# Optimization experiments

Measured on AMD Instinct MI355X. Metric: run time of the kernel, lower is better.

## Reference

```python
import jax, jax.numpy as jnp
import numpy as np

B, F, V, D = 16384, 16, 100000, 16  # batch, n_fields, vocab, embed_dim; dims = F*D = 256
EPS = 1e-5


def _bn(x, g, b):
    # torch.nn.BatchNorm1d in training mode: biased batch variance
    m = x.mean(0)
    v = x.var(0)
    return g * (x - m) * jax.lax.rsqrt(v + EPS) + b


def setup_inputs() -> dict:
    ks = iter(jax.random.split(jax.random.key(0), 40))

    def rn(shape, s=0.05):
        return jax.random.normal(next(ks), shape, jnp.float32) * s

    return {
        "feat_ids": jax.random.randint(next(ks), (B, F), 0, V, jnp.int32),
        "domain_ids": jax.random.randint(next(ks), (B,), 0, 3, jnp.int32),
        "emb": rn((F, V, D), 0.1),
        "hW0": rn((256, 128)), "hb0": jnp.zeros(128), "hg0": jnp.ones(128), "hbe0": jnp.zeros(128),
        "hW1": rn((128, 64)), "hb1": jnp.zeros(64), "hg1": jnp.ones(64), "hbe1": jnp.zeros(64),
        "hW2": rn((64, 1024)), "hb2": jnp.zeros(1024), "hg2": jnp.ones(1024), "hbe2": jnp.zeros(1024),
        "cw": rn((3, 256)), "cb": jnp.zeros((3, 256)),
        "mW0": rn((256, 512)), "mb0": jnp.zeros(512), "mg0": jnp.ones(512), "mbe0": jnp.zeros(512),
        "mW1": rn((512, 256)), "mb1": jnp.zeros(256), "mg1": jnp.ones(256), "mbe1": jnp.zeros(256),
        "u0": rn((256, 32)), "u1": rn((32, 32)), "v0": rn((32, 32)), "v1": rn((32, 256)),
        "ab0": jnp.zeros(32), "ab1": jnp.zeros(256),
        "gamma1": jnp.ones(256), "bias1": jnp.zeros(256),
        "lw": rn((512,)), "lb": jnp.zeros(1),
    }


def _forward(feat_ids, emb, hW0, hb0, hg0, hbe0, hW1, hb1, hg1, hbe1,
             hW2, hb2, hg2, hbe2, cw, cb, mW0, mb0, mg0, mbe0,
             mW1, mb1, mg1, mbe1, u0, u1, v0, v1, ab0, ab1,
             gamma1, bias1, lw, lb):
    b, f = feat_ids.shape
    # EmbeddingLayer(squeeze_dim=True): per-field lookup then concat -> [B, F*D]
    e = emb[jnp.arange(f)[None, :], feat_ids].reshape(b, -1)
    h = e
    for W, bb, g, be in ((hW0, hb0, hg0, hbe0), (hW1, hb1, hg1, hbe1), (hW2, hb2, hg2, hbe2)):
        h = jax.nn.relu(_bn(h @ W + bb, g, be))
    k = u1.shape[0]
    H = h.reshape(b, k, k)  # [B, k, k]
    # CrossNetwork: x_{l+1} = x0 * (x_l . w_l) + b_l + x_l
    x = e
    for i in range(cw.shape[0]):
        x = e * (x @ cw[i])[:, None] + cb[i] + x
    cn_out = x  # [B, 256]
    m = e
    for W, bb, g, be in ((mW0, mb0, mg0, mbe0), (mW1, mb1, mg1, mbe1)):
        m = jax.nn.relu(_bn(m @ W + bb, g, be))
    # hyper low-rank adapter: einsum('mi,bij,jn->bmn') applied lazily so the
    # [B,256,32] per-sample weight is never materialized (associativity)
    t = jax.nn.sigmoid(jnp.einsum('bi,bij->bj', m @ u0, H) @ v0 + ab0)   # [B, 32]
    t = jnp.einsum('bi,bij->bj', t @ u1, H) @ v1 + ab1                    # [B, 256]
    mu = t.mean(0)
    var = t.var(0, ddof=1)  # torch.var default is unbiased
    m = gamma1 * (t - mu) / jnp.sqrt(var + EPS) + bias1 + m  # norm + residual
    y = jnp.concatenate([cn_out, m], axis=1) @ lw + lb[0]     # LR head
    # Every domain branch computes identical values (shared weights, full-batch
    # input, dropout p=0), so the torch.where domain-select is the identity.
    return jax.nn.sigmoid(y)  # [B]


def reference(feat_ids, domain_ids, emb, hW0, hb0, hg0, hbe0, hW1, hb1, hg1, hbe1,
              hW2, hb2, hg2, hbe2, cw, cb, mW0, mb0, mg0, mbe0,
              mW1, mb1, mg1, mbe1, u0, u1, v0, v1, ab0, ab1,
              gamma1, bias1, lw, lb):
    return _forward(feat_ids, emb, hW0, hb0, hg0, hbe0, hW1, hb1, hg1, hbe1,
                    hW2, hb2, hg2, hbe2, cw, cb, mW0, mb0, mg0, mbe0,
                    mW1, mb1, mg1, mbe1, u0, u1, v0, v1, ab0, ab1,
                    gamma1, bias1, lw, lb)
```

## Files before the change

kernel.cpp:

```cpp
#include <hip/hip_runtime.h>

typedef unsigned short u16;
typedef __attribute__((ext_vector_type(8))) short bf16x8;
typedef __attribute__((ext_vector_type(4))) float f32x4;
#define BATCH 16384

__device__ __forceinline__ float b2f(u16 u){ unsigned int i=((unsigned int)u)<<16; float f; __builtin_memcpy(&f,&i,4); return f; }
__device__ __forceinline__ u16 f2b(float f){ unsigned int x; __builtin_memcpy(&x,&f,4); unsigned int r=(x + 0x7fffu + ((x>>16)&1u))>>16; return (u16)r; }

__global__ __launch_bounds__(256) void prep_kernel(float* __restrict__ S,
                                                   const float* __restrict__ hb0, const float* __restrict__ mb0,
                                                   float* __restrict__ catb,
                                                   const float* __restrict__ w0, const float* __restrict__ w1,
                                                   const float* __restrict__ w2, const float* __restrict__ w3,
                                                   const float* __restrict__ w4, const float* __restrict__ w5,
                                                   const float* __restrict__ w6,
                                                   u16* __restrict__ catWt, u16* __restrict__ t1,
                                                   u16* __restrict__ t2, u16* __restrict__ t4,
                                                   u16* __restrict__ t5, u16* __restrict__ t6,
                                                   const int* __restrict__ ids,
                                                   const float* __restrict__ emb,
                                                   u16* __restrict__ e){
  int blk = blockIdx.x;
  int tid = threadIdx.x;
  if (blk < 18){
    int i = blk*256 + tid;
    if (i < 4480) S[i] = 0.f;
  } else if (blk == 18){
    for (int i = tid; i < 640; i += 256) catb[i] = (i < 128) ? hb0[i] : mb0[i-128];
  } else if (blk < 1523){
    int c = blk - 19;
    if (c < 640){        int idx=c*256+tid;        int n=idx>>8, k=idx&255;
                         catWt[idx] = f2b(n<128 ? w0[k*128+n] : w3[k*512+(n-128)]); }
    else if (c < 672){   int idx=(c-640)*256+tid;  t1[idx]=f2b(w1[(idx%128)*64   + idx/128]); }
    else if (c < 928){   int idx=(c-672)*256+tid;  t2[idx]=f2b(w2[(idx%64)*1024  + idx/64]);  }
    else if (c < 1440){  int idx=(c-928)*256+tid;  t4[idx]=f2b(w4[(idx%512)*256  + idx/512]); }
    else if (c < 1472){  int idx=(c-1440)*256+tid; t5[idx]=f2b(w5[(idx%256)*32   + idx/256]); }
    else {               int idx=(c-1472)*256+tid; t6[idx]=f2b(w6[(idx%32)*256   + idx/32]);  }
  } else {
    int g = blk - 1523;
    int b = g*16 + (tid >> 4), f = tid & 15;
    int id = ids[b*16 + f];
    const float4* src = (const float4*)(emb + ((size_t)f*100000 + (size_t)id)*16);
    float4 v0 = src[0], v1 = src[1], v2 = src[2], v3 = src[3];
    u16 o[16] = { f2b(v0.x),f2b(v0.y),f2b(v0.z),f2b(v0.w), f2b(v1.x),f2b(v1.y),f2b(v1.z),f2b(v1.w),
                  f2b(v2.x),f2b(v2.y),f2b(v2.z),f2b(v2.w), f2b(v3.x),f2b(v3.y),f2b(v3.z),f2b(v3.w) };
    uint4 p0, p1; __builtin_memcpy(&p0, &o[0], 16); __builtin_memcpy(&p1, &o[8], 16);
    uint4* dst = (uint4*)(e + (size_t)b*256 + f*16);
    dst[0] = p0; dst[1] = p1;
  }
}

template<int BK>
__device__ __forceinline__ void gemm_body(const u16* __restrict__ A,
                                          const u16* __restrict__ Wt,
                                          const float* __restrict__ bias,
                                          u16* __restrict__ Ca,
                                          u16* __restrict__ Cb,
                                          int Nsplit,
                                          const float* __restrict__ asums,
                                          const float* __restrict__ asumsq,
                                          const float* __restrict__ ag,
                                          const float* __restrict__ abe,
                                          float* __restrict__ sums,
                                          float* __restrict__ sumsq,
                                          int N, int K, int n0, int m0,
                                          u16* lds, float* bnS, float* bnB){
  constexpr int STR = BK + 8;
  constexpr int EPT = BK/4;
  u16* As = lds;
  u16* Bs = lds + 64*STR;
  int tid = threadIdx.x;
  int lane = tid & 63, w = tid >> 6, quad = lane >> 4, m16 = lane & 15;
  int srow = tid >> 2, skoff = (tid & 3)*EPT;
  if (asums != nullptr){
    for (int k = tid; k < K; k += 256){
      float mean = asums[k] * (1.f/(float)BATCH);
      float var  = asumsq[k] * (1.f/(float)BATCH) - mean*mean;
      float sc   = ag[k] * rsqrtf(var + 1e-5f);
      bnS[k] = sc;
      bnB[k] = abe[k] - mean*sc;
    }
    __syncthreads();
  }
  f32x4 acc[4] = {};
  int ng = n0 + srow;
  uint4 a0, a1, b0, b1;
  {
    const u16* ap = A + (size_t)(m0+srow)*K + skoff;
    a0 = *(const uint4*)ap;
    if (EPT == 16) a1 = *(const uint4*)(ap + 8);
    if (ng < N){
      const u16* bp = Wt + (size_t)ng*K + skoff;
      b0 = *(const uint4*)bp;
      if (EPT == 16) b1 = *(const uint4*)(bp + 8);
    } else { b0 = make_uint4(0u,0u,0u,0u); b1 = b0; }
  }
  for (int k0 = 0; k0 < K; k0 += BK){
    u16 at[EPT];
    __builtin_memcpy(at, &a0, 16);
    if (EPT == 16) __builtin_memcpy(at+8, &a1, 16);
    if (asums != nullptr){
#pragma unroll
      for (int j=0;j<EPT;j++){
        float v = b2f(at[j]) * bnS[k0+skoff+j] + bnB[k0+skoff+j];
        at[j] = f2b(v > 0.f ? v : 0.f);
      }
    }
    uint4 s0, s1;
    __builtin_memcpy(&s0, at, 16);
    *(uint4*)&As[srow*STR + skoff] = s0;
    if (EPT == 16){ __builtin_memcpy(&s1, at+8, 16); *(uint4*)&As[srow*STR + skoff + 8] = s1; }
    *(uint4*)&Bs[srow*STR + skoff] = b0;
    if (EPT == 16) *(uint4*)&Bs[srow*STR + skoff + 8] = b1;
    if (k0 + BK < K){
      const u16* ap = A + (size_t)(m0+srow)*K + k0 + BK + skoff;
      a0 = *(const uint4*)ap;
      if (EPT == 16) a1 = *(const uint4*)(ap + 8);
      if (ng < N){
        const u16* bp = Wt + (size_t)ng*K + k0 + BK + skoff;
        b0 = *(const uint4*)bp;
        if (EPT == 16) b1 = *(const uint4*)(bp + 8);
      }
    }
    __syncthreads();
#pragma unroll
    for (int sub=0; sub<BK/32; sub++){
      bf16x8 bfrag = *(bf16x8*)&Bs[(w*16 + m16)*STR + sub*32 + quad*8];
#pragma unroll
      for (int mc=0;mc<4;mc++){
        bf16x8 afrag = *(bf16x8*)&As[(mc*16 + m16)*STR + sub*32 + quad*8];
        acc[mc] = __builtin_amdgcn_mfma_f32_16x16x32_bf16(afrag, bfrag, acc[mc], 0, 0, 0);
      }
    }
    __syncthreads();
  }
  int cw = n0 + w*16 + m16;
  float bvv = (bias != nullptr && cw < N) ? bias[cw] : 0.f;
  float cs = 0.f, cq = 0.f;
  u16* Cs = lds;
#pragma unroll
  for (int mc=0;mc<4;mc++)
#pragma unroll
    for (int r=0;r<4;r++){
      float v = acc[mc][r] + bvv;
      cs += v; cq += v*v;
      Cs[(mc*16 + quad*4 + r)*72 + w*16 + m16] = f2b(v);
    }
  if (sums != nullptr){
    cs += __shfl_xor(cs, 16, 64); cs += __shfl_xor(cs, 32, 64);
    cq += __shfl_xor(cq, 16, 64); cq += __shfl_xor(cq, 32, 64);
    if (quad == 0 && cw < N){ atomicAdd(&sums[cw], cs); atomicAdd(&sumsq[cw], cq); }
  }
  __syncthreads();
  int row = tid >> 2, c4 = (tid & 3)*16;
  int cg = n0 + c4;
  if (cg < N){
    u16* outp; int stride, colbase;
    if (Cb != nullptr && n0 >= Nsplit){ outp = Cb; stride = N - Nsplit; colbase = cg - Nsplit; }
    else if (Cb != nullptr){            outp = Ca; stride = Nsplit;     colbase = cg; }
    else {                              outp = Ca; stride = N;          colbase = cg; }
    uint4 p0 = *(uint4*)&Cs[row*72 + c4];
    uint4 p1 = *(uint4*)&Cs[row*72 + c4 + 8];
    *(uint4*)(outp + (size_t)(m0+row)*stride + colbase) = p0;
    *(uint4*)(outp + (size_t)(m0+row)*stride + colbase + 8) = p1;
  }
}

template<int BK>
__global__ __launch_bounds__(256) void gemm_mfma(const u16* __restrict__ A,
                                                 const u16* __restrict__ Wt,
                                                 const float* __restrict__ bias,
                                                 u16* __restrict__ Ca,
                                                 u16* __restrict__ Cb,
                                                 int Nsplit,
                                                 const float* __restrict__ asums,
                                                 const float* __restrict__ asumsq,
                                                 const float* __restrict__ ag,
                                                 const float* __restrict__ abe,
                                                 float* __restrict__ sums,
                                                 float* __restrict__ sumsq,
                                                 int N, int K){
  constexpr int STR = BK + 8;
  __shared__ u16 lds[64*STR*2];
  __shared__ float bnS[512], bnB[512];
  gemm_body<BK>(A, Wt, bias, Ca, Cb, Nsplit, asums, asumsq, ag, abe,
                sums, sumsq, N, K, blockIdx.x*64, blockIdx.y*64, lds, bnS, bnB);
}

__global__ __launch_bounds__(256) void gemm_dual(
    const u16* __restrict__ A1, const u16* __restrict__ Wt1, const float* __restrict__ b1,
    u16* __restrict__ C1,
    const float* __restrict__ as1, const float* __restrict__ aq1,
    const float* __restrict__ g1v, const float* __restrict__ be1,
    float* __restrict__ s1, float* __restrict__ q1, int N1, int K1, int nb1, int nblk1,
    const u16* __restrict__ A2, const u16* __restrict__ Wt2, const float* __restrict__ b2,
    u16* __restrict__ C2,
    const float* __restrict__ as2, const float* __restrict__ aq2,
    const float* __restrict__ g2v, const float* __restrict__ be2,
    float* __restrict__ s2, float* __restrict__ q2, int N2, int K2, int nblk2){
  constexpr int STR = 64 + 8;
  __shared__ u16 lds[64*STR*2];
  __shared__ float bnS[512], bnB[512];
  int blk = blockIdx.x;
  if (blk < nb1){
    int n0 = (blk % nblk1)*64, m0 = (blk / nblk1)*64;
    gemm_body<64>(A1, Wt1, b1, C1, nullptr, 0, as1, aq1, g1v, be1,
                  s1, q1, N1, K1, n0, m0, lds, bnS, bnB);
  } else {
    int q = blk - nb1;
    int n0 = (q % nblk2)*64, m0 = (q / nblk2)*64;
    gemm_body<64>(A2, Wt2, b2, C2, nullptr, 0, as2, aq2, g2v, be2,
                  s2, q2, N2, K2, n0, m0, lds, bnS, bnB);
  }
}

#define HSTR 1056
__global__ __launch_bounds__(512) void adapter_core(const u16* __restrict__ H,
                                                    const u16* __restrict__ Mout,
                                                    const u16* __restrict__ u0t,
                                                    const float* __restrict__ v0,
                                                    const float* __restrict__ u1,
                                                    const float* __restrict__ ab0,
                                                    const float* __restrict__ hsums,
                                                    const float* __restrict__ hsumsq,
                                                    const float* __restrict__ hg,
                                                    const float* __restrict__ hbe,
                                                    const float* __restrict__ msums,
                                                    const float* __restrict__ msumsq,
                                                    const float* __restrict__ mg,
                                                    const float* __restrict__ mbe,
                                                    u16* __restrict__ Z2){
  __shared__ __align__(16) u16 Hs[16*HSTR];
  __shared__ float bnS[1024], bnB[1024];
  __shared__ __align__(8) u16 v0s[1024], u1s[1024];
  __shared__ float mS[256], mB[256];
  __shared__ float PT[512], QS[512];
  __shared__ float ab0s[32];
  int tid = threadIdx.x;
  int r = tid >> 5, j = tid & 31;
  size_t row0 = (size_t)blockIdx.x * 16;
  u16* aS = Hs;

  for (int k = tid; k < 1024; k += 512){
    float mean = hsums[k] * (1.f/(float)BATCH);
    float var  = hsumsq[k] * (1.f/(float)BATCH) - mean*mean;
    float sc   = hg[k] * rsqrtf(var + 1e-5f);
    bnS[k] = sc; bnB[k] = hbe[k] - mean*sc;
  }
  if (tid < 256){
    float4 a = *(const float4*)(v0 + tid*4);
    ushort4 pa = { f2b(a.x), f2b(a.y), f2b(a.z), f2b(a.w) };
    *(ushort4*)&v0s[tid*4] = pa;
    float4 b4 = *(const float4*)(u1 + tid*4);
    ushort4 pb = { f2b(b4.x), f2b(b4.y), f2b(b4.z), f2b(b4.w) };
    *(ushort4*)&u1s[tid*4] = pb;
  } else {
    int c = tid - 256;
    float mean = msums[c] * (1.f/(float)BATCH);
    float var  = msumsq[c] * (1.f/(float)BATCH) - mean*mean;
    float sc   = mg[c] * rsqrtf(var + 1e-5f);
    mS[c] = sc; mB[c] = mbe[c] - mean*sc;
  }
  {
    int el = tid*8;
    uint4 mv = *(const uint4*)(Mout + row0*256 + el);
    *(uint4*)&aS[el] = mv;
  }
  if (tid < 32) ab0s[tid] = ab0[tid];
  __syncthreads();

  {
    int el = tid*8, col = el & 255;
    u16 mt[8]; __builtin_memcpy(mt, &aS[el], 16);
#pragma unroll
    for (int q=0;q<8;q++){
      float v = b2f(mt[q]) * mS[col+q] + mB[col+q];
      mt[q] = f2b(v > 0.f ? v : 0.f);
    }
    uint4 so; __builtin_memcpy(&so, mt, 16);
    *(uint4*)&aS[el] = so;
  }
  __syncthreads();

  {
    float acc = 0.f;
    for (int k8 = 0; k8 < 256; k8 += 8){
      uint4 vu = *(const uint4*)(u0t + j*256 + k8);
      uint4 va; __builtin_memcpy(&va, &aS[r*256 + k8], 16);
      u16 ta[8], tu[8]; __builtin_memcpy(ta, &va, 16); __builtin_memcpy(tu, &vu, 16);
#pragma unroll
      for (int q=0;q<8;q++) acc += b2f(ta[q]) * b2f(tu[q]);
    }
    PT[tid] = acc;
  }
  __syncthreads();

#pragma unroll
  for (int it=0; it<4; it++){
    int el = it*4096 + tid*8;
    int rr = el >> 10, col = el & 1023;
    uint4 hv = *(const uint4*)(H + row0*1024 + el);
    u16 ht[8]; __builtin_memcpy(ht, &hv, 16);
#pragma unroll
    for (int q=0;q<8;q++){
      float v = b2f(ht[q]) * bnS[col+q] + bnB[col+q];
      ht[q] = f2b(v > 0.f ? v : 0.f);
    }
    uint4 so; __builtin_memcpy(&so, ht, 16);
    *(uint4*)&Hs[rr*HSTR + col] = so;
  }
  __syncthreads();

  float acc = 0.f;
#pragma unroll
  for (int i=0;i<32;i++) acc += PT[r*32+i] * b2f(Hs[r*HSTR + i*32 + j]);
  QS[tid] = acc;
  __syncthreads();
  acc = ab0s[j];
#pragma unroll
  for (int i=0;i<32;i++) acc += QS[r*32+i] * b2f(v0s[i*32+j]);
  PT[tid] = 1.f / (1.f + __expf(-acc));
  __syncthreads();
  acc = 0.f;
#pragma unroll
  for (int i=0;i<32;i++) acc += PT[r*32+i] * b2f(u1s[i*32+j]);
  QS[tid] = acc;
  __syncthreads();
  acc = 0.f;
#pragma unroll
  for (int i=0;i<32;i++) acc += QS[r*32+i] * b2f(Hs[r*HSTR + i*32 + j]);
  Z2[(row0 + r)*32 + j] = f2b(acc);
}

__global__ __launch_bounds__(256) void final_kernel(const u16* __restrict__ e,
                                                    const float* __restrict__ cw,
                                                    const float* __restrict__ cb,
                                                    const u16* __restrict__ t,
                                                    const u16* __restrict__ mo,
                                                    const float* __restrict__ tsums,
                                                    const float* __restrict__ tsumsq,
                                                    const float* __restrict__ tg,
                                                    const float* __restrict__ tbe,
                                                    const float* __restrict__ msums,
                                                    const float* __restrict__ msumsq,
                                                    const float* __restrict__ mg,
                                                    const float* __restrict__ mbe,
                                                    const float* __restrict__ lw,
                                                    const float* __restrict__ lb,
                                                    float* __restrict__ out){
  __shared__ float tS[256], tB[256], mS[256], mB[256];
  int tid = threadIdx.x;
  {
    int c = tid;
    float mean = tsums[c] * (1.f/(float)BATCH);
    float var  = (tsumsq[c] - mean*mean*(float)BATCH) * (1.f/(float)(BATCH-1));
    float sc   = tg[c] * rsqrtf(var + 1e-5f);
    tS[c] = sc; tB[c] = tbe[c] - mean*sc;
    float mmean = msums[c] * (1.f/(float)BATCH);
    float mvar  = msumsq[c] * (1.f/(float)BATCH) - mmean*mmean;
    float msc   = mg[c] * rsqrtf(mvar + 1e-5f);
    mS[c] = msc; mB[c] = mbe[c] - mmean*msc;
  }
  __syncthreads();
  int wave = tid >> 6, lane = tid & 63;
  int b = blockIdx.x*4 + wave;
  int n4 = lane*4;
  ushort4 ev = *(const ushort4*)(e + (size_t)b*256 + n4);
  float ec[4] = { b2f(ev.x), b2f(ev.y), b2f(ev.z), b2f(ev.w) };
  float x[4]  = { ec[0], ec[1], ec[2], ec[3] };
  for (int i=0;i<3;i++){
    float p = 0.f;
#pragma unroll
    for (int q=0;q<4;q++) p += x[q] * cw[i*256 + n4 + q];
#pragma unroll
    for (int o=1;o<64;o<<=1) p += __shfl_xor(p, o, 64);
#pragma unroll
    for (int q=0;q<4;q++) x[q] = ec[q]*p + cb[i*256 + n4 + q] + x[q];
  }
  ushort4 tv = *(const ushort4*)(t  + (size_t)b*256 + n4);
  ushort4 mv = *(const ushort4*)(mo + (size_t)b*256 + n4);
  float ta[4] = { b2f(tv.x), b2f(tv.y), b2f(tv.z), b2f(tv.w) };
  float ma[4] = { b2f(mv.x), b2f(mv.y), b2f(mv.z), b2f(mv.w) };
  float p = 0.f;
#pragma unroll
  for (int q=0;q<4;q++){
    int n = n4 + q;
    p += x[q] * lw[n];
    float mr = ma[q]*mS[n] + mB[n];
    mr = mr > 0.f ? mr : 0.f;
    float mf = tS[n]*ta[q] + tB[n] + mr;
    p += mf * lw[256 + n];
  }
#pragma unroll
  for (int o=32;o>0;o>>=1) p += __shfl_down(p, o, 64);
  if (lane == 0){
    float y = p + lb[0];
    out[b] = 1.f / (1.f + __expf(-y));
  }
}

extern "C" void kernel_launch(void* const* d_in, const int* in_sizes, int n_in,
                              void* d_out, int out_size, void* d_ws, size_t ws_size,
                              hipStream_t stream) {
  const int B = BATCH;
  const int*   feat = (const int*)d_in[0];
  const float* emb  = (const float*)d_in[2];
  const float* hW0 = (const float*)d_in[3],  *hb0 = (const float*)d_in[4],  *hg0 = (const float*)d_in[5],  *hbe0 = (const float*)d_in[6];
  const float* hW1 = (const float*)d_in[7],  *hb1 = (const float*)d_in[8],  *hg1 = (const float*)d_in[9],  *hbe1 = (const float*)d_in[10];
  const float* hW2 = (const float*)d_in[11], *hb2 = (const float*)d_in[12], *hg2 = (const float*)d_in[13], *hbe2 = (const float*)d_in[14];
  const float* cw  = (const float*)d_in[15], *cb  = (const float*)d_in[16];
  const float* mW0 = (const float*)d_in[17], *mb0 = (const float*)d_in[18], *mg0 = (const float*)d_in[19], *mbe0 = (const float*)d_in[20];
  const float* mW1 = (const float*)d_in[21], *mb1 = (const float*)d_in[22], *mg1 = (const float*)d_in[23], *mbe1 = (const float*)d_in[24];
  const float* u0  = (const float*)d_in[25], *u1  = (const float*)d_in[26];
  const float* v0  = (const float*)d_in[27], *v1  = (const float*)d_in[28];
  const float* ab0 = (const float*)d_in[29], *ab1 = (const float*)d_in[30];
  const float* gamma1 = (const float*)d_in[31], *bias1 = (const float*)d_in[32];
  const float* lw  = (const float*)d_in[33], *lb = (const float*)d_in[34];
  float* out = (float*)d_out;

  char* base = (char*)d_ws;
  const size_t MB = 1024*1024;
  u16* H    = (u16*)(base);
  u16* e    = (u16*)(base + 32*MB);
  u16* Y0   = (u16*)(base + 40*MB);
  u16* Y1   = (u16*)(base + 44*MB);
  u16* M0   = (u16*)(base + 48*MB);
  u16* Mout = (u16*)(base + 64*MB);
  u16* T    = (u16*)(base + 72*MB);
  u16* Z2   = (u16*)(base + 80*MB);
  u16* catWt= (u16*)(base + 88*MB);
  u16* hW1t = catWt + 163840;
  u16* hW2t = hW1t + 8192;
  u16* mW1t = hW2t + 65536;
  u16* u0t  = mW1t + 131072;
  u16* v1t  = u0t + 8192;
  float* catb = (float*)(v1t + 8192);
  float* S    = catb + 640;

  prep_kernel<<<2547, 256, 0, stream>>>(S, hb0, mb0, catb,
                                        hW0, hW1, hW2, mW0, mW1, u0, v1,
                                        catWt, hW1t, hW2t, mW1t, u0t, v1t,
                                        feat, emb, e);

  gemm_mfma<64><<<dim3(10, B/64), 256, 0, stream>>>(e, catWt, catb, Y0, M0, 128,
      nullptr, nullptr, nullptr, nullptr, S+0, S+640, 640, 256);

  gemm_dual<<<1280, 256, 0, stream>>>(
      Y0, hW1t, hb1, Y1, S+0, S+640, hg0, hbe0, S+1280, S+1344, 64, 128, 256, 1,
      M0, mW1t, mb1, Mout, S+128, S+768, mg0, mbe0, S+3456, S+3712, 256, 512, 4);

  gemm_mfma<64><<<dim3(16, B/64), 256, 0, stream>>>(Y1, hW2t, hb2, H, nullptr, 0,
      S+1280, S+1344, hg1, hbe1, S+1408, S+2432, 1024, 64);

  adapter_core<<<B/16, 512, 0, stream>>>(H, Mout, u0t, v0, u1, ab0,
      S+1408, S+2432, hg2, hbe2, S+3456, S+3712, mg1, mbe1, Z2);
  gemm_mfma<32><<<dim3(4, B/64), 256, 0, stream>>>(Z2, v1t, ab1, T, nullptr, 0,
      nullptr, nullptr, nullptr, nullptr, S+3968, S+4224, 256, 32);

  final_kernel<<<B/4, 256, 0, stream>>>(e, cw, cb, T, Mout,
      S+3968, S+4224, gamma1, bias1,
      S+3456, S+3712, mg1, mbe1, lw, lb, out);
}
```

Before: 324.3 us.

## Fuse all stages into one persistent cooperative kernel with grid syncs

```diff
diff --git a/kernel.cpp b/kernel.cpp
--- a/kernel.cpp
+++ b/kernel.cpp
@@ -1,55 +1,16 @@
 #include <hip/hip_runtime.h>
+#include <hip/hip_cooperative_groups.h>
+
+namespace cg = cooperative_groups;
 
 typedef unsigned short u16;
 typedef __attribute__((ext_vector_type(8))) short bf16x8;
 typedef __attribute__((ext_vector_type(4))) float f32x4;
 #define BATCH 16384
+#define HSTR 1056
 
 __device__ __forceinline__ float b2f(u16 u){ unsigned int i=((unsigned int)u)<<16; float f; __builtin_memcpy(&f,&i,4); return f; }
 __device__ __forceinline__ u16 f2b(float f){ unsigned int x; __builtin_memcpy(&x,&f,4); unsigned int r=(x + 0x7fffu + ((x>>16)&1u))>>16; return (u16)r; }
-
-__global__ __launch_bounds__(256) void prep_kernel(float* __restrict__ S,
-                                                   const float* __restrict__ hb0, const float* __restrict__ mb0,
-                                                   float* __restrict__ catb,
-                                                   const float* __restrict__ w0, const float* __restrict__ w1,
-                                                   const float* __restrict__ w2, const float* __restrict__ w3,
-                                                   const float* __restrict__ w4, const float* __restrict__ w5,
-                                                   const float* __restrict__ w6,
-                                                   u16* __restrict__ catWt, u16* __restrict__ t1,
-                                                   u16* __restrict__ t2, u16* __restrict__ t4,
-                                                   u16* __restrict__ t5, u16* __restrict__ t6,
-                                                   const int* __restrict__ ids,
-                                                   const float* __restrict__ emb,
-                                                   u16* __restrict__ e){
-  int blk = blockIdx.x;
-  int tid = threadIdx.x;
-  if (blk < 18){
-    int i = blk*256 + tid;
-    if (i < 4480) S[i] = 0.f;
-  } else if (blk == 18){
-    for (int i = tid; i < 640; i += 256) catb[i] = (i < 128) ? hb0[i] : mb0[i-128];
-  } else if (blk < 1523){
-    int c = blk - 19;
-    if (c < 640){        int idx=c*256+tid;        int n=idx>>8, k=idx&255;
-                         catWt[idx] = f2b(n<128 ? w0[k*128+n] : w3[k*512+(n-128)]); }
-    else if (c < 672){   int idx=(c-640)*256+tid;  t1[idx]=f2b(w1[(idx%128)*64   + idx/128]); }
-    else if (c < 928){   int idx=(c-672)*256+tid;  t2[idx]=f2b(w2[(idx%64)*1024  + idx/64]);  }
-    else if (c < 1440){  int idx=(c-928)*256+tid;  t4[idx]=f2b(w4[(idx%512)*256  + idx/512]); }
-    else if (c < 1472){  int idx=(c-1440)*256+tid; t5[idx]=f2b(w5[(idx%256)*32   + idx/256]); }
-    else {               int idx=(c-1472)*256+tid; t6[idx]=f2b(w6[(idx%32)*256   + idx/32]);  }
-  } else {
-    int g = blk - 1523;
-    int b = g*16 + (tid >> 4), f = tid & 15;
-    int id = ids[b*16 + f];
-    const float4* src = (const float4*)(emb + ((size_t)f*100000 + (size_t)id)*16);
-    float4 v0 = src[0], v1 = src[1], v2 = src[2], v3 = src[3];
-    u16 o[16] = { f2b(v0.x),f2b(v0.y),f2b(v0.z),f2b(v0.w), f2b(v1.x),f2b(v1.y),f2b(v1.z),f2b(v1.w),
-                  f2b(v2.x),f2b(v2.y),f2b(v2.z),f2b(v2.w), f2b(v3.x),f2b(v3.y),f2b(v3.z),f2b(v3.w) };
-    uint4 p0, p1; __builtin_memcpy(&p0, &o[0], 16); __builtin_memcpy(&p1, &o[8], 16);
-    uint4* dst = (uint4*)(e + (size_t)b*256 + f*16);
-    dst[0] = p0; dst[1] = p1;
-  }
-}
 
 template<int BK>
 __device__ __forceinline__ void gemm_body(const u16* __restrict__ A,
@@ -167,298 +128,323 @@
   }
 }
 
-template<int BK>
-__global__ __launch_bounds__(256) void gemm_mfma(const u16* __restrict__ A,
-                                                 const u16* __restrict__ Wt,
-                                                 const float* __restrict__ bias,
-                                                 u16* __restrict__ Ca,
-                                                 u16* __restrict__ Cb,
-                                                 int Nsplit,
-                                                 const float* __restrict__ asums,
-                                                 const float* __restrict__ asumsq,
-                                                 const float* __restrict__ ag,
-                                                 const float* __restrict__ abe,
-                                                 float* __restrict__ sums,
-                                                 float* __restrict__ sumsq,
-                                                 int N, int K){
-  constexpr int STR = BK + 8;
-  __shared__ u16 lds[64*STR*2];
-  __shared__ float bnS[512], bnB[512];
-  gemm_body<BK>(A, Wt, bias, Ca, Cb, Nsplit, asums, asumsq, ag, abe,
-                sums, sumsq, N, K, blockIdx.x*64, blockIdx.y*64, lds, bnS, bnB);
-}
-
-__global__ __launch_bounds__(256) void gemm_dual(
-    const u16* __restrict__ A1, const u16* __restrict__ Wt1, const float* __restrict__ b1,
-    u16* __restrict__ C1,
-    const float* __restrict__ as1, const float* __restrict__ aq1,
-    const float* __restrict__ g1v, const float* __restrict__ be1,
-    float* __restrict__ s1, float* __restrict__ q1, int N1, int K1, int nb1, int nblk1,
-    const u16* __restrict__ A2, const u16* __restrict__ Wt2, const float* __restrict__ b2,
-    u16* __restrict__ C2,
-    const float* __restrict__ as2, const float* __restrict__ aq2,
-    const float* __restrict__ g2v, const float* __restrict__ be2,
-    float* __restrict__ s2, float* __restrict__ q2, int N2, int K2, int nblk2){
-  constexpr int STR = 64 + 8;
-  __shared__ u16 lds[64*STR*2];
-  __shared__ float bnS[512], bnB[512];
-  int blk = blockIdx.x;
-  if (blk < nb1){
-    int n0 = (blk % nblk1)*64, m0 = (blk / nblk1)*64;
-    gemm_body<64>(A1, Wt1, b1, C1, nullptr, 0, as1, aq1, g1v, be1,
-                  s1, q1, N1, K1, n0, m0, lds, bnS, bnB);
-  } else {
-    int q = blk - nb1;
-    int n0 = (q % nblk2)*64, m0 = (q / nblk2)*64;
-    gemm_body<64>(A2, Wt2, b2, C2, nullptr, 0, as2, aq2, g2v, be2,
-                  s2, q2, N2, K2, n0, m0, lds, bnS, bnB);
-  }
-}
-
-#define HSTR 1056
-__global__ __launch_bounds__(512) void adapter_core(const u16* __restrict__ H,
-                                                    const u16* __restrict__ Mout,
-                                                    const u16* __restrict__ u0t,
-                                                    const float* __restrict__ v0,
-                                                    const float* __restrict__ u1,
-                                                    const float* __restrict__ ab0,
-                                                    const float* __restrict__ hsums,
-                                                    const float* __restrict__ hsumsq,
-                                                    const float* __restrict__ hg,
-                                                    const float* __restrict__ hbe,
-                                                    const float* __restrict__ msums,
-                                                    const float* __restrict__ msumsq,
-                                                    const float* __restrict__ mg,
-                                                    const float* __restrict__ mbe,
-                                                    u16* __restrict__ Z2){
-  __shared__ __align__(16) u16 Hs[16*HSTR];
-  __shared__ float bnS[1024], bnB[1024];
-  __shared__ __align__(8) u16 v0s[1024], u1s[1024];
-  __shared__ float mS[256], mB[256];
-  __shared__ float PT[512], QS[512];
-  __shared__ float ab0s[32];
-  int tid = threadIdx.x;
-  int r = tid >> 5, j = tid & 31;
-  size_t row0 = (size_t)blockIdx.x * 16;
-  u16* aS = Hs;
-
-  for (int k = tid; k < 1024; k += 512){
-    float mean = hsums[k] * (1.f/(float)BATCH);
-    float var  = hsumsq[k] * (1.f/(float)BATCH) - mean*mean;
-    float sc   = hg[k] * rsqrtf(var + 1e-5f);
-    bnS[k] = sc; bnB[k] = hbe[k] - mean*sc;
-  }
-  if (tid < 256){
-    float4 a = *(const float4*)(v0 + tid*4);
-    ushort4 pa = { f2b(a.x), f2b(a.y), f2b(a.z), f2b(a.w) };
-    *(ushort4*)&v0s[tid*4] = pa;
-    float4 b4 = *(const float4*)(u1 + tid*4);
-    ushort4 pb = { f2b(b4.x), f2b(b4.y), f2b(b4.z), f2b(b4.w) };
-    *(ushort4*)&u1s[tid*4] = pb;
-  } else {
-    int c = tid - 256;
-    float mean = msums[c] * (1.f/(float)BATCH);
-    float var  = msumsq[c] * (1.f/(float)BATCH) - mean*mean;
-    float sc   = mg[c] * rsqrtf(var + 1e-5f);
-    mS[c] = sc; mB[c] = mbe[c] - mean*sc;
-  }
+struct MegaArgs {
+  const int* feat; const float* emb;
+  const float *hb0, *mb0;
+  const float *hW0, *hW1, *hW2, *mW0, *mW1, *u0w, *v1w;
+  const float *hg0, *hbe0, *hb1, *hg1, *hbe1, *hb2, *hg2, *hbe2;
+  const float *mb1, *mg0, *mbe0, *mg1, *mbe1;
+  const float *v0, *u1, *ab0, *ab1, *gamma1, *bias1, *cw, *cb, *lw, *lb;
+  u16 *H, *e, *Y0, *Y1, *M0, *Mout, *T;
+  u16 *catWt, *hW1t, *hW2t, *mW1t, *u0t, *v1t;
+  float *catb, *S, *hSg, *hBg, *mSg, *mBg;
+  float* out;
+};
+
+__global__ __launch_bounds__(256, 4) void mega_kernel(MegaArgs a){
+  __shared__ __align__(16) char smem[23424];
+  cg::grid_group gg = cg::this_grid();
+  const int tid = threadIdx.x;
+  const int bid = blockIdx.x;
+  const int nb  = gridDim.x;
+
   {
-    int el = tid*8;
-    uint4 mv = *(const uint4*)(Mout + row0*256 + el);
-    *(uint4*)&aS[el] = mv;
-  }
-  if (tid < 32) ab0s[tid] = ab0[tid];
-  __syncthreads();
+    int gi = bid*256 + tid;
+    if (gi < 4480) a.S[gi] = 0.f;
+    else if (gi < 5120){ int i = gi - 4480; a.catb[i] = (i < 128) ? a.hb0[i] : a.mb0[i-128]; }
+    for (int c = bid; c < 1504; c += nb){
+      if (c < 640){        int idx=c*256+tid;        int n=idx>>8, k=idx&255;
+                           a.catWt[idx] = f2b(n<128 ? a.hW0[k*128+n] : a.mW0[k*512+(n-128)]); }
+      else if (c < 672){   int idx=(c-640)*256+tid;  a.hW1t[idx]=f2b(a.hW1[(idx%128)*64   + idx/128]); }
+      else if (c < 928){   int idx=(c-672)*256+tid;  a.hW2t[idx]=f2b(a.hW2[(idx%64)*1024  + idx/64]);  }
+      else if (c < 1440){  int idx=(c-928)*256+tid;  a.mW1t[idx]=f2b(a.mW1[(idx%512)*256  + idx/512]); }
+      else if (c < 1472){  int idx=(c-1440)*256+tid; a.u0t[idx]=f2b(a.u0w[(idx%256)*32   + idx/256]); }
+      else {               int idx=(c-1472)*256+tid; a.v1t[idx]=f2b(a.v1w[(idx%32)*256   + idx/32]);  }
+    }
+    for (int g = bid; g < 1024; g += nb){
+      int b = g*16 + (tid >> 4), f = tid & 15;
+      int id = a.feat[b*16 + f];
+      const float4* src = (const float4*)(a.emb + ((size_t)f*100000 + (size_t)id)*16);
+      float4 v0 = src[0], v1 = src[1], v2 = src[2], v3 = src[3];
+      u16 o[16] = { f2b(v0.x),f2b(v0.y),f2b(v0.z),f2b(v0.w), f2b(v1.x),f2b(v1.y),f2b(v1.z),f2b(v1.w),
+                    f2b(v2.x),f2b(v2.y),f2b(v2.z),f2b(v2.w), f2b(v3.x),f2b(v3.y),f2b(v3.z),f2b(v3.w) };
+      uint4 p0, p1; __builtin_memcpy(&p0, &o[0], 16); __builtin_memcpy(&p1, &o[8], 16);
+      uint4* dst = (uint4*)(a.e + (size_t)b*256 + f*16);
+      dst[0] = p0; dst[1] = p1;
+    }
+  }
+  gg.sync();
+
+  u16*  glds = (u16*)smem;
+  float* bnS = (float*)(smem + 18432);
+  float* bnB = (float*)(smem + 18432 + 2048);
+
+  for (int t = bid; t < 2560; t += nb){
+    __syncthreads();
+    gemm_body<64>(a.e, a.catWt, a.catb, a.Y0, a.M0, 128,
+                  nullptr, nullptr, nullptr, nullptr,
+                  a.S+0, a.S+640, 640, 256, (t%10)*64, (t/10)*64, glds, bnS, bnB);
+  }
+  gg.sync();
+
+  for (int t = bid; t < 1280; t += nb){
+    __syncthreads();
+    if (t < 256){
+      gemm_body<64>(a.Y0, a.hW1t, a.hb1, a.Y1, nullptr, 0,
+                    a.S+0, a.S+640, a.hg0, a.hbe0,
+                    a.S+1280, a.S+1344, 64, 128, 0, t*64, glds, bnS, bnB);
+    } else {
+      int q = t - 256;
+      gemm_body<64>(a.M0, a.mW1t, a.mb1, a.Mout, nullptr, 0,
+                    a.S+128, a.S+768, a.mg0, a.mbe0,
+                    a.S+3456, a.S+3712, 256, 512, (q%4)*64, (q/4)*64, glds, bnS, bnB);
+    }
+  }
+  gg.sync();
+
+  for (int t = bid; t < 4096; t += nb){
+    __syncthreads();
+    gemm_body<64>(a.Y1, a.hW2t, a.hb2, a.H, nullptr, 0,
+                  a.S+1280, a.S+1344, a.hg1, a.hbe1,
+                  a.S+1408, a.S+2432, 1024, 64, (t%16)*64, (t/16)*64, glds, bnS, bnB);
+  }
+  gg.sync();
+
+  if (bid < 4){
+    int i = bid*256 + tid;
+    float mean = a.S[1408+i] * (1.f/(float)BATCH);
+    float var  = a.S[2432+i] * (1.f/(float)BATCH) - mean*mean;
+    float sc   = a.hg2[i] * rsqrtf(var + 1e-5f);
+    a.hSg[i] = sc; a.hBg[i] = a.hbe2[i] - mean*sc;
+    if (i < 256){
+      float mmean = a.S[3456+i] * (1.f/(float)BATCH);
+      float mvar  = a.S[3712+i] * (1.f/(float)BATCH) - mmean*mmean;
+      float msc   = a.mg1[i] * rsqrtf(mvar + 1e-5f);
+      a.mSg[i] = msc; a.mBg[i] = a.mbe1[i] - mmean*msc;
+    }
+  }
+  gg.sync();
 
   {
-    int el = tid*8, col = el & 255;
-    u16 mt[8]; __builtin_memcpy(mt, &aS[el], 16);
-#pragma unroll
-    for (int q=0;q<8;q++){
-      float v = b2f(mt[q]) * mS[col+q] + mB[col+q];
-      mt[q] = f2b(v > 0.f ? v : 0.f);
-    }
-    uint4 so; __builtin_memcpy(&so, mt, 16);
-    *(uint4*)&aS[el] = so;
-  }
-  __syncthreads();
+    u16* Hs   = (u16*)smem;
+    u16* v0s  = (u16*)(smem + 16896);
+    u16* u1s  = (u16*)(smem + 18944);
+    float* PT = (float*)(smem + 20992);
+    float* QS = (float*)(smem + 22016);
+    float* ab0s = (float*)(smem + 23040);
+    int r = tid >> 5, j = tid & 31;
+    {
+      float4 av = *(const float4*)(a.v0 + tid*4);
+      ushort4 pa = { f2b(av.x), f2b(av.y), f2b(av.z), f2b(av.w) };
+      *(ushort4*)&v0s[tid*4] = pa;
+      float4 b4 = *(const float4*)(a.u1 + tid*4);
+      ushort4 pb = { f2b(b4.x), f2b(b4.y), f2b(b4.z), f2b(b4.w) };
+      *(ushort4*)&u1s[tid*4] = pb;
+      if (tid < 32) ab0s[tid] = a.ab0[tid];
+    }
+    __syncthreads();
+    for (int t = bid; t < 2048; t += nb){
+      size_t row0 = (size_t)t * 8;
+      const u16* Hb = a.H + row0*1024 + tid*8;
+      uint4 h0 = *(const uint4*)(Hb);
+      uint4 h1 = *(const uint4*)(Hb + 2048);
+      uint4 h2 = *(const uint4*)(Hb + 4096);
+      uint4 h3 = *(const uint4*)(Hb + 6144);
+      {
+        int el = tid*8, col = el & 255;
+        uint4 mv = *(const uint4*)(a.Mout + row0*256 + el);
+        float4 s0 = *(const float4*)(a.mSg + col), s1 = *(const float4*)(a.mSg + col + 4);
+        float4 bb0 = *(const float4*)(a.mBg + col), bb1 = *(const float4*)(a.mBg + col + 4);
+        float sv[8] = { s0.x,s0.y,s0.z,s0.w, s1.x,s1.y,s1.z,s1.w };
+        float bv[8] = { bb0.x,bb0.y,bb0.z,bb0.w, bb1.x,bb1.y,bb1.z,bb1.w };
+        u16 mt[8]; __builtin_memcpy(mt, &mv, 16);
+#pragma unroll
+        for (int q=0;q<8;q++){
+          float v = b2f(mt[q]) * sv[q] + bv[q];
+          mt[q] = f2b(v > 0.f ? v : 0.f);
+        }
+        uint4 so; __builtin_memcpy(&so, mt, 16);
+        *(uint4*)&Hs[el] = so;
+      }
+      {
+        float accp = 0.f;
+        for (int k8 = 0; k8 < 256; k8 += 8){
+          uint4 vu = *(const uint4*)(a.u0t + j*256 + k8);
+          uint4 va; __builtin_memcpy(&va, &Hs[r*256 + k8], 16);
+          u16 ta[8], tu[8]; __builtin_memcpy(ta, &va, 16); __builtin_memcpy(tu, &vu, 16);
+#pragma unroll
+          for (int q=0;q<8;q++) accp += b2f(ta[q]) * b2f(tu[q]);
+        }
+        PT[tid] = accp;
+      }
+      __syncthreads();
+#pragma unroll
+      for (int it=0; it<4; it++){
+        int el2 = it*2048 + tid*8, rr = el2 >> 10, col2 = el2 & 1023;
+        uint4 hv = (it==0)?h0:(it==1)?h1:(it==2)?h2:h3;
+        float4 s0 = *(const float4*)(a.hSg + col2), s1 = *(const float4*)(a.hSg + col2 + 4);
+        float4 bb0 = *(const float4*)(a.hBg + col2), bb1 = *(const float4*)(a.hBg + col2 + 4);
+        float sv[8] = { s0.x,s0.y,s0.z,s0.w, s1.x,s1.y,s1.z,s1.w };
+        float bv[8] = { bb0.x,bb0.y,bb0.z,bb0.w, bb1.x,bb1.y,bb1.z,bb1.w };
+        u16 ht[8]; __builtin_memcpy(ht, &hv, 16);
+#pragma unroll
+        for (int q=0;q<8;q++){
+          float v = b2f(ht[q]) * sv[q] + bv[q];
+          ht[q] = f2b(v > 0.f ? v : 0.f);
+        }
+        uint4 so; __builtin_memcpy(&so, ht, 16);
+        *(uint4*)&Hs[rr*HSTR + col2] = so;
+      }
+      __syncthreads();
+      float acc = 0.f;
+#pragma unroll
+      for (int i=0;i<32;i++) acc += PT[r*32+i] * b2f(Hs[r*HSTR + i*32 + j]);
+      QS[tid] = acc;
+      acc = ab0s[j];
+#pragma unroll
+      for (int i=0;i<32;i++) acc += QS[r*32+i] * b2f(v0s[i*32+j]);
+      PT[tid] = 1.f / (1.f + __expf(-acc));
+      acc = 0.f;
+#pragma unroll
+      for (int i=0;i<32;i++) acc += PT[r*32+i] * b2f(u1s[i*32+j]);
+      QS[tid] = acc;
+      acc = 0.f;
+#pragma unroll
+      for (int i=0;i<32;i++) acc += QS[r*32+i] * b2f(Hs[r*HSTR + i*32 + j]);
+      PT[tid] = b2f(f2b(acc));
+      __syncthreads();
+      u16* Ts = Hs;
+#pragma unroll
+      for (int c8=0;c8<8;c8++){
+        int c = j + 32*c8;
+        const u16* vp = a.v1t + (size_t)c*32;
+        uint4 q0 = *(const uint4*)vp, q1 = *(const uint4*)(vp+8);
+        uint4 q2 = *(const uint4*)(vp+16), q3 = *(const uint4*)(vp+24);
+        u16 tv[32];
+        __builtin_memcpy(tv, &q0, 16);    __builtin_memcpy(tv+8, &q1, 16);
+        __builtin_memcpy(tv+16, &q2, 16); __builtin_memcpy(tv+24, &q3, 16);
+        float tt = a.ab1[c];
+#pragma unroll
+        for (int k=0;k<32;k++) tt += PT[r*32+k] * b2f(tv[k]);
+        Ts[r*264 + c] = f2b(tt);
+      }
+      __syncthreads();
+      {
+        float s = 0.f, qq = 0.f;
+#pragma unroll
+        for (int rr=0;rr<8;rr++){ float v = b2f(Ts[rr*264 + tid]); s += v; qq += v*v; }
+        atomicAdd(&a.S[3968+tid], s); atomicAdd(&a.S[4224+tid], qq);
+      }
+      {
+        int rr = tid >> 5, cb2 = (tid & 31)*8;
+        uint4 pv = *(uint4*)&Ts[rr*264 + cb2];
+        *(uint4*)(a.T + (row0 + rr)*256 + cb2) = pv;
+      }
+      __syncthreads();
+    }
+  }
+  gg.sync();
 
   {
-    float acc = 0.f;
-    for (int k8 = 0; k8 < 256; k8 += 8){
-      uint4 vu = *(const uint4*)(u0t + j*256 + k8);
-      uint4 va; __builtin_memcpy(&va, &aS[r*256 + k8], 16);
-      u16 ta[8], tu[8]; __builtin_memcpy(ta, &va, 16); __builtin_memcpy(tu, &vu, 16);
-#pragma unroll
-      for (int q=0;q<8;q++) acc += b2f(ta[q]) * b2f(tu[q]);
-    }
-    PT[tid] = acc;
-  }
-  __syncthreads();
-
-#pragma unroll
-  for (int it=0; it<4; it++){
-    int el = it*4096 + tid*8;
-    int rr = el >> 10, col = el & 1023;
-    uint4 hv = *(const uint4*)(H + row0*1024 + el);
-    u16 ht[8]; __builtin_memcpy(ht, &hv, 16);
-#pragma unroll
-    for (int q=0;q<8;q++){
-      float v = b2f(ht[q]) * bnS[col+q] + bnB[col+q];
-      ht[q] = f2b(v > 0.f ? v : 0.f);
-    }
-    uint4 so; __builtin_memcpy(&so, ht, 16);
-    *(uint4*)&Hs[rr*HSTR + col] = so;
-  }
-  __syncthreads();
-
-  float acc = 0.f;
-#pragma unroll
-  for (int i=0;i<32;i++) acc += PT[r*32+i] * b2f(Hs[r*HSTR + i*32 + j]);
-  QS[tid] = acc;
-  __syncthreads();
-  acc = ab0s[j];
-#pragma unroll
-  for (int i=0;i<32;i++) acc += QS[r*32+i] * b2f(v0s[i*32+j]);
-  PT[tid] = 1.f / (1.f + __expf(-acc));
-  __syncthreads();
-  acc = 0.f;
-#pragma unroll
-  for (int i=0;i<32;i++) acc += PT[r*32+i] * b2f(u1s[i*32+j]);
-  QS[tid] = acc;
-  __syncthreads();
-  acc = 0.f;
-#pragma unroll
-  for (int i=0;i<32;i++) acc += QS[r*32+i] * b2f(Hs[r*HSTR + i*32 + j]);
-  Z2[(row0 + r)*32 + j] = f2b(acc);
-}
-
-__global__ __launch_bounds__(256) void final_kernel(const u16* __restrict__ e,
-                                                    const float* __restrict__ cw,
-                                                    const float* __restrict__ cb,
-                                                    const u16* __restrict__ t,
-                                                    const u16* __restrict__ mo,
-                                                    const float* __restrict__ tsums,
-                                                    const float* __restrict__ tsumsq,
-                                                    const float* __restrict__ tg,
-                                                    const float* __restrict__ tbe,
-                                                    const float* __restrict__ msums,
-                                                    const float* __restrict__ msumsq,
-                                                    const float* __restrict__ mg,
-                                                    const float* __restrict__ mbe,
-                                                    const float* __restrict__ lw,
-                                                    const float* __restrict__ lb,
-                                                    float* __restrict__ out){
-  __shared__ float tS[256], tB[256], mS[256], mB[256];
-  int tid = threadIdx.x;
-  {
-    int c = tid;
-    float mean = tsums[c] * (1.f/(float)BATCH);
-    float var  = (tsumsq[c] - mean*mean*(float)BATCH) * (1.f/(float)(BATCH-1));
-    float sc   = tg[c] * rsqrtf(var + 1e-5f);
-    tS[c] = sc; tB[c] = tbe[c] - mean*sc;
-    float mmean = msums[c] * (1.f/(float)BATCH);
-    float mvar  = msumsq[c] * (1.f/(float)BATCH) - mmean*mmean;
-    float msc   = mg[c] * rsqrtf(mvar + 1e-5f);
-    mS[c] = msc; mB[c] = mbe[c] - mmean*msc;
-  }
-  __syncthreads();
-  int wave = tid >> 6, lane = tid & 63;
-  int b = blockIdx.x*4 + wave;
-  int n4 = lane*4;
-  ushort4 ev = *(const ushort4*)(e + (size_t)b*256 + n4);
-  float ec[4] = { b2f(ev.x), b2f(ev.y), b2f(ev.z), b2f(ev.w) };
-  float x[4]  = { ec[0], ec[1], ec[2], ec[3] };
-  for (int i=0;i<3;i++){
-    float p = 0.f;
-#pragma unroll
-    for (int q=0;q<4;q++) p += x[q] * cw[i*256 + n4 + q];
-#pragma unroll
-    for (int o=1;o<64;o<<=1) p += __shfl_xor(p, o, 64);
-#pragma unroll
-    for (int q=0;q<4;q++) x[q] = ec[q]*p + cb[i*256 + n4 + q] + x[q];
-  }
-  ushort4 tv = *(const ushort4*)(t  + (size_t)b*256 + n4);
-  ushort4 mv = *(const ushort4*)(mo + (size_t)b*256 + n4);
-  float ta[4] = { b2f(tv.x), b2f(tv.y), b2f(tv.z), b2f(tv.w) };
-  float ma[4] = { b2f(mv.x), b2f(mv.y), b2f(mv.z), b2f(mv.w) };
-  float p = 0.f;
-#pragma unroll
-  for (int q=0;q<4;q++){
-    int n = n4 + q;
-    p += x[q] * lw[n];
-    float mr = ma[q]*mS[n] + mB[n];
-    mr = mr > 0.f ? mr : 0.f;
-    float mf = tS[n]*ta[q] + tB[n] + mr;
-    p += mf * lw[256 + n];
-  }
-#pragma unroll
-  for (int o=32;o>0;o>>=1) p += __shfl_down(p, o, 64);
-  if (lane == 0){
-    float y = p + lb[0];
-    out[b] = 1.f / (1.f + __expf(-y));
+    float* tS = (float*)smem;
+    float* tB = tS + 256;
+    float* mS = tB + 256;
+    float* mB = mS + 256;
+    {
+      int c = tid;
+      float mean = a.S[3968+c] * (1.f/(float)BATCH);
+      float var  = (a.S[4224+c] - mean*mean*(float)BATCH) * (1.f/(float)(BATCH-1));
+      float sc   = a.gamma1[c] * rsqrtf(var + 1e-5f);
+      tS[c] = sc; tB[c] = a.bias1[c] - mean*sc;
+      mS[c] = a.mSg[c]; mB[c] = a.mBg[c];
+    }
+    __syncthreads();
+    int wave = tid >> 6, lane = tid & 63, n4 = lane*4;
+    for (int g = bid; g < 4096; g += nb){
+      int b = g*4 + wave;
+      ushort4 ev = *(const ushort4*)(a.e + (size_t)b*256 + n4);
+      float ec[4] = { b2f(ev.x), b2f(ev.y), b2f(ev.z), b2f(ev.w) };
+      float x[4]  = { ec[0], ec[1], ec[2], ec[3] };
+      for (int i=0;i<3;i++){
+        float p = 0.f;
+#pragma unroll
+        for (int q=0;q<4;q++) p += x[q] * a.cw[i*256 + n4 + q];
+#pragma unroll
+        for (int o=1;o<64;o<<=1) p += __shfl_xor(p, o, 64);
+#pragma unroll
+        for (int q=0;q<4;q++) x[q] = ec[q]*p + a.cb[i*256 + n4 + q] + x[q];
+      }
+      ushort4 tv = *(const ushort4*)(a.T  + (size_t)b*256 + n4);
+      ushort4 mv = *(const ushort4*)(a.Mout + (size_t)b*256 + n4);
+      float ta[4] = { b2f(tv.x), b2f(tv.y), b2f(tv.z), b2f(tv.w) };
+      float ma[4] = { b2f(mv.x), b2f(mv.y), b2f(mv.z), b2f(mv.w) };
+      float p = 0.f;
+#pragma unroll
+      for (int q=0;q<4;q++){
+        int n = n4 + q;
+        p += x[q] * a.lw[n];
+        float mr = ma[q]*mS[n] + mB[n];
+        mr = mr > 0.f ? mr : 0.f;
+        float mf = tS[n]*ta[q] + tB[n] + mr;
+        p += mf * a.lw[256 + n];
+      }
+#pragma unroll
+      for (int o=32;o>0;o>>=1) p += __shfl_down(p, o, 64);
+      if (lane == 0){
+        float y = p + a.lb[0];
+        a.out[b] = 1.f / (1.f + __expf(-y));
+      }
+    }
   }
 }
 
 extern "C" void kernel_launch(void* const* d_in, const int* in_sizes, int n_in,
                               void* d_out, int out_size, void* d_ws, size_t ws_size,
                               hipStream_t stream) {
-  const int B = BATCH;
-  const int*   feat = (const int*)d_in[0];
-  const float* emb  = (const float*)d_in[2];
-  const float* hW0 = (const float*)d_in[3],  *hb0 = (const float*)d_in[4],  *hg0 = (const float*)d_in[5],  *hbe0 = (const float*)d_in[6];
-  const float* hW1 = (const float*)d_in[7],  *hb1 = (const float*)d_in[8],  *hg1 = (const float*)d_in[9],  *hbe1 = (const float*)d_in[10];
-  const float* hW2 = (const float*)d_in[11], *hb2 = (const float*)d_in[12], *hg2 = (const float*)d_in[13], *hbe2 = (const float*)d_in[14];
-  const float* cw  = (const float*)d_in[15], *cb  = (const float*)d_in[16];
-  const float* mW0 = (const float*)d_in[17], *mb0 = (const float*)d_in[18], *mg0 = (const float*)d_in[19], *mbe0 = (const float*)d_in[20];
-  const float* mW1 = (const float*)d_in[21], *mb1 = (const float*)d_in[22], *mg1 = (const float*)d_in[23], *mbe1 = (const float*)d_in[24];
-  const float* u0  = (const float*)d_in[25], *u1  = (const float*)d_in[26];
-  const float* v0  = (const float*)d_in[27], *v1  = (const float*)d_in[28];
-  const float* ab0 = (const float*)d_in[29], *ab1 = (const float*)d_in[30];
-  const float* gamma1 = (const float*)d_in[31], *bias1 = (const float*)d_in[32];
-  const float* lw  = (const float*)d_in[33], *lb = (const float*)d_in[34];
-  float* out = (float*)d_out;
+  MegaArgs a;
+  a.feat = (const int*)d_in[0];
+  a.emb  = (const float*)d_in[2];
+  a.hW0 = (const float*)d_in[3];  a.hb0 = (const float*)d_in[4];  a.hg0 = (const float*)d_in[5];  a.hbe0 = (const float*)d_in[6];
+  a.hW1 = (const float*)d_in[7];  a.hb1 = (const float*)d_in[8];  a.hg1 = (const float*)d_in[9];  a.hbe1 = (const float*)d_in[10];
+  a.hW2 = (const float*)d_in[11]; a.hb2 = (const float*)d_in[12]; a.hg2 = (const float*)d_in[13]; a.hbe2 = (const float*)d_in[14];
+  a.cw  = (const float*)d_in[15]; a.cb  = (const float*)d_in[16];
+  a.mW0 = (const float*)d_in[17]; a.mb0 = (const float*)d_in[18]; a.mg0 = (const float*)d_in[19]; a.mbe0 = (const float*)d_in[20];
+  a.mW1 = (const float*)d_in[21]; a.mb1 = (const float*)d_in[22]; a.mg1 = (const float*)d_in[23]; a.mbe1 = (const float*)d_in[24];
+  a.u0w = (const float*)d_in[25]; a.u1  = (const float*)d_in[26];
+  a.v0  = (const float*)d_in[27]; a.v1w = (const float*)d_in[28];
+  a.ab0 = (const float*)d_in[29]; a.ab1 = (const float*)d_in[30];
+  a.gamma1 = (const float*)d_in[31]; a.bias1 = (const float*)d_in[32];
+  a.lw  = (const float*)d_in[33]; a.lb = (const float*)d_in[34];
+  a.out = (float*)d_out;
 
   char* base = (char*)d_ws;
   const size_t MB = 1024*1024;
-  u16* H    = (u16*)(base);
-  u16* e    = (u16*)(base + 32*MB);
-  u16* Y0   = (u16*)(base + 40*MB);
-  u16* Y1   = (u16*)(base + 44*MB);
-  u16* M0   = (u16*)(base + 48*MB);
-  u16* Mout = (u16*)(base + 64*MB);
-  u16* T    = (u16*)(base + 72*MB);
-  u16* Z2   = (u16*)(base + 80*MB);
-  u16* catWt= (u16*)(base + 88*MB);
-  u16* hW1t = catWt + 163840;
-  u16* hW2t = hW1t + 8192;
-  u16* mW1t = hW2t + 65536;
-  u16* u0t  = mW1t + 131072;
-  u16* v1t  = u0t + 8192;
-  float* catb = (float*)(v1t + 8192);
-  float* S    = catb + 640;
-
-  prep_kernel<<<2547, 256, 0, stream>>>(S, hb0, mb0, catb,
-                                        hW0, hW1, hW2, mW0, mW1, u0, v1,
-                                        catWt, hW1t, hW2t, mW1t, u0t, v1t,
-                                        feat, emb, e);
-
-  gemm_mfma<64><<<dim3(10, B/64), 256, 0, stream>>>(e, catWt, catb, Y0, M0, 128,
-      nullptr, nullptr, nullptr, nullptr, S+0, S+640, 640, 256);
-
-  gemm_dual<<<1280, 256, 0, stream>>>(
-      Y0, hW1t, hb1, Y1, S+0, S+640, hg0, hbe0, S+1280, S+1344, 64, 128, 256, 1,
-      M0, mW1t, mb1, Mout, S+128, S+768, mg0, mbe0, S+3456, S+3712, 256, 512, 4);
-
-  gemm_mfma<64><<<dim3(16, B/64), 256, 0, stream>>>(Y1, hW2t, hb2, H, nullptr, 0,
-      S+1280, S+1344, hg1, hbe1, S+1408, S+2432, 1024, 64);
-
-  adapter_core<<<B/16, 512, 0, stream>>>(H, Mout, u0t, v0, u1, ab0,
-      S+1408, S+2432, hg2, hbe2, S+3456, S+3712, mg1, mbe1, Z2);
-  gemm_mfma<32><<<dim3(4, B/64), 256, 0, stream>>>(Z2, v1t, ab1, T, nullptr, 0,
-      nullptr, nullptr, nullptr, nullptr, S+3968, S+4224, 256, 32);
-
-  final_kernel<<<B/4, 256, 0, stream>>>(e, cw, cb, T, Mout,
-      S+3968, S+4224, gamma1, bias1,
-      S+3456, S+3712, mg1, mbe1, lw, lb, out);
+  a.H    = (u16*)(base);
+  a.e    = (u16*)(base + 32*MB);
+  a.Y0   = (u16*)(base + 40*MB);
+  a.Y1   = (u16*)(base + 44*MB);
+  a.M0   = (u16*)(base + 48*MB);
+  a.Mout = (u16*)(base + 64*MB);
+  a.T    = (u16*)(base + 72*MB);
+  float* TZ = (float*)(base + 80*MB);
+  a.hSg = TZ; a.hBg = TZ + 1024; a.mSg = TZ + 2048; a.mBg = TZ + 2304;
+  a.catWt = (u16*)(base + 88*MB);
+  a.hW1t = a.catWt + 163840;
+  a.hW2t = a.hW1t + 8192;
+  a.mW1t = a.hW2t + 65536;
+  a.u0t  = a.mW1t + 131072;
+  a.v1t  = a.u0t + 8192;
+  a.catb = (float*)(a.v1t + 8192);
+  a.S    = a.catb + 640;
+
+  int maxb = 0;
+  hipError_t qe = hipOccupancyMaxActiveBlocksPerMultiprocessor(&maxb,
+                    reinterpret_cast<const void*>(mega_kernel), 256, 0);
+  if (qe != hipSuccess || maxb < 1) maxb = 2;
+  if (maxb > 4) maxb = 4;
+  int nblocks = 256 * maxb;
+
+  void* kargs[] = { (void*)&a };
+  hipLaunchCooperativeKernel(reinterpret_cast<const void*>(mega_kernel),
+                             dim3(nblocks), dim3(256), kargs, 0, stream);
 }
```

After: 809.9 us. +149.7%, slower.
